# Optimization experiments

Measured on AMD Instinct MI355X. Metric: run time of the kernel, lower is better.

## Reference

```python
import jax, jax.numpy as jnp
import numpy as np

IN_DIM, HID_DIM, OUT_DIM, N_EXP = 3, 20, 3, 5
BATCH = 1 << 20


def setup_inputs() -> dict:
    key = jax.random.key(0)
    ks = jax.random.split(key, 8)
    s_in = 1.0 / np.sqrt(IN_DIM)
    s_hid = 1.0 / np.sqrt(HID_DIM)
    return {
        "x": jax.random.normal(ks[0], (BATCH, IN_DIM), dtype=jnp.float32),
        # stacked expert params: fc1 [E, in, hid], fc2 [E, hid, out]
        "W1": jax.random.uniform(ks[1], (N_EXP, IN_DIM, HID_DIM), jnp.float32, -s_in, s_in),
        "b1": jax.random.uniform(ks[2], (N_EXP, HID_DIM), jnp.float32, -s_in, s_in),
        "W2": jax.random.uniform(ks[3], (N_EXP, HID_DIM, OUT_DIM), jnp.float32, -s_hid, s_hid),
        "b2": jax.random.uniform(ks[4], (N_EXP, OUT_DIM), jnp.float32, -s_hid, s_hid),
        # gate Linear(in, n_experts)
        "Wg": jax.random.uniform(ks[5], (IN_DIM, N_EXP), jnp.float32, -s_in, s_in),
        "bg": jax.random.uniform(ks[6], (N_EXP,), jnp.float32, -s_in, s_in),
    }


def reference(x, W1, b1, W2, b2, Wg, bg):
    # all experts as one batched GEMM: h [B, E, hid]
    h = jax.nn.relu(jnp.einsum("bi,eih->beh", x, W1) + b1)
    expert_out = jnp.einsum("beh,eho->beo", h, W2) + b2  # [B, E, out]
    gate = jax.nn.softmax(x @ Wg + bg, axis=-1)           # [B, E]
    mixed = jnp.einsum("be,beo->bo", gate, expert_out)    # [B, out]
    return (mixed, gate)
```

## Files before the change

### kernel.cpp

```cpp
#include <hip/hip_runtime.h>

#define IN_DIM  3
#define HID_DIM 20
#define OUT_DIM 3
#define N_EXP   5
#define ELEMS   4
#define BLOCK   256
#define SPAN    (BLOCK * ELEMS)


__global__ __launch_bounds__(BLOCK) void moe_kernel(
    const float* __restrict__ x,
    const float* __restrict__ W1,
    const float* __restrict__ b1,
    const float* __restrict__ W2,
    const float* __restrict__ b2,
    const float* __restrict__ Wg,
    const float* __restrict__ bg,
    float* __restrict__ out,
    int B)
{
    __shared__ float sIO[SPAN * N_EXP];

    const int t = threadIdx.x;
    const long long blockBase = (long long)blockIdx.x * SPAN;
    float* __restrict__ mixed_out = out;
    float* __restrict__ gate_out  = out + (long long)B * OUT_DIM;

    if (blockBase + SPAN <= (long long)B) {
        const size_t bb = (size_t)blockBase;

        {
            const float4* g4 = reinterpret_cast<const float4*>(x + bb * IN_DIM);
            float4* s4 = reinterpret_cast<float4*>(sIO);
            #pragma unroll
            for (int k = 0; k < 3; ++k) s4[t + k * BLOCK] = g4[t + k * BLOCK];
        }
        __syncthreads();

        float xf[ELEMS * IN_DIM];
        {
            const float4* s4 = reinterpret_cast<const float4*>(sIO);
            #pragma unroll
            for (int k = 0; k < 3; ++k) {
                float4 v = s4[3 * t + k];
                xf[4 * k + 0] = v.x; xf[4 * k + 1] = v.y;
                xf[4 * k + 2] = v.z; xf[4 * k + 3] = v.w;
            }
        }
        __syncthreads();

        float gate[ELEMS][N_EXP];
        #pragma unroll
        for (int c = 0; c < ELEMS; ++c) {
            float lg[N_EXP]; float s = 0.f;
            #pragma unroll
            for (int e = 0; e < N_EXP; ++e) {
                float v = bg[e];
                #pragma unroll
                for (int i = 0; i < IN_DIM; ++i)
                    v = fmaf(xf[c * IN_DIM + i], Wg[i * N_EXP + e], v);
                v = __expf(v);
                lg[e] = v; s += v;
            }
            const float inv = 1.0f / s;
            #pragma unroll
            for (int e = 0; e < N_EXP; ++e) gate[c][e] = lg[e] * inv;
        }
        {
            float4* s4 = reinterpret_cast<float4*>(sIO);
            float g[ELEMS * N_EXP];
            #pragma unroll
            for (int c = 0; c < ELEMS; ++c)
                #pragma unroll
                for (int e = 0; e < N_EXP; ++e) g[c * N_EXP + e] = gate[c][e];
            #pragma unroll
            for (int k = 0; k < 5; ++k)
                s4[5 * t + k] = make_float4(g[4 * k + 0], g[4 * k + 1],
                                            g[4 * k + 2], g[4 * k + 3]);
        }
        __syncthreads();

        {
            float4* o4 = reinterpret_cast<float4*>(gate_out + bb * N_EXP);
            const float4* s4 = reinterpret_cast<const float4*>(sIO);
            #pragma unroll
            for (int k = 0; k < 5; ++k) o4[t + k * BLOCK] = s4[t + k * BLOCK];
        }

        float mix[ELEMS][OUT_DIM];
        #pragma unroll
        for (int c = 0; c < ELEMS; ++c) {
            #pragma unroll
            for (int k = 0; k < OUT_DIM; ++k) {
                float m = 0.f;
                #pragma unroll
                for (int e = 0; e < N_EXP; ++e)
                    m = fmaf(gate[c][e], b2[e * OUT_DIM + k], m);
                mix[c][k] = m;
            }
        }
        #pragma unroll
        for (int e = 0; e < N_EXP; ++e) {
            #pragma unroll
            for (int j = 0; j < HID_DIM; ++j) {
                const float w10 = W1[(e * IN_DIM + 0) * HID_DIM + j];
                const float w11 = W1[(e * IN_DIM + 1) * HID_DIM + j];
                const float w12 = W1[(e * IN_DIM + 2) * HID_DIM + j];
                const float bb1 = b1[e * HID_DIM + j];
                const float w20 = W2[(e * HID_DIM + j) * OUT_DIM + 0];
                const float w21 = W2[(e * HID_DIM + j) * OUT_DIM + 1];
                const float w22 = W2[(e * HID_DIM + j) * OUT_DIM + 2];
                #pragma unroll
                for (int c = 0; c < ELEMS; ++c) {
                    float h = fmaf(xf[c * IN_DIM + 2], w12,
                              fmaf(xf[c * IN_DIM + 1], w11,
                              fmaf(xf[c * IN_DIM + 0], w10, bb1)));
                    h = fmaxf(h, 0.f);
                    const float hg = h * gate[c][e];
                    mix[c][0] = fmaf(hg, w20, mix[c][0]);
                    mix[c][1] = fmaf(hg, w21, mix[c][1]);
                    mix[c][2] = fmaf(hg, w22, mix[c][2]);
                }
            }
        }
        __syncthreads();

        {
            float4* s4 = reinterpret_cast<float4*>(sIO);
            float m[ELEMS * OUT_DIM];
            #pragma unroll
            for (int c = 0; c < ELEMS; ++c)
                #pragma unroll
                for (int k = 0; k < OUT_DIM; ++k) m[c * OUT_DIM + k] = mix[c][k];
            #pragma unroll
            for (int k = 0; k < 3; ++k)
                s4[3 * t + k] = make_float4(m[4 * k + 0], m[4 * k + 1],
                                            m[4 * k + 2], m[4 * k + 3]);
        }
        __syncthreads();

        {
            float4* o4 = reinterpret_cast<float4*>(mixed_out + bb * OUT_DIM);
            const float4* s4 = reinterpret_cast<const float4*>(sIO);
            #pragma unroll
            for (int k = 0; k < 3; ++k) o4[t + k * BLOCK] = s4[t + k * BLOCK];
        }
    } else {
        for (int c = 0; c < ELEMS; ++c) {
            const long long bidx = blockBase + (long long)c * BLOCK + t;
            if (bidx >= (long long)B) continue;
            float xv[IN_DIM];
            for (int i = 0; i < IN_DIM; ++i) xv[i] = x[bidx * IN_DIM + i];

            float lg[N_EXP]; float s = 0.f;
            for (int e = 0; e < N_EXP; ++e) {
                float v = bg[e];
                for (int i = 0; i < IN_DIM; ++i)
                    v = fmaf(xv[i], Wg[i * N_EXP + e], v);
                v = __expf(v); lg[e] = v; s += v;
            }
            const float inv = 1.0f / s;
            for (int e = 0; e < N_EXP; ++e) lg[e] *= inv;

            float mixv[OUT_DIM] = {0.f, 0.f, 0.f};
            for (int e = 0; e < N_EXP; ++e) {
                for (int k = 0; k < OUT_DIM; ++k)
                    mixv[k] = fmaf(lg[e], b2[e * OUT_DIM + k], mixv[k]);
                for (int j = 0; j < HID_DIM; ++j) {
                    float h = b1[e * HID_DIM + j];
                    for (int i = 0; i < IN_DIM; ++i)
                        h = fmaf(xv[i], W1[(e * IN_DIM + i) * HID_DIM + j], h);
                    h = fmaxf(h, 0.f);
                    const float hg = h * lg[e];
                    for (int k = 0; k < OUT_DIM; ++k)
                        mixv[k] = fmaf(hg, W2[(e * HID_DIM + j) * OUT_DIM + k], mixv[k]);
                }
            }
            for (int k = 0; k < OUT_DIM; ++k)
                mixed_out[bidx * OUT_DIM + k] = mixv[k];
            for (int e = 0; e < N_EXP; ++e)
                gate_out[bidx * N_EXP + e] = lg[e];
        }
    }
}

extern "C" void kernel_launch(void* const* d_in, const int* in_sizes, int n_in,
                              void* d_out, int out_size, void* d_ws, size_t ws_size,
                              hipStream_t stream) {
    const float* x  = (const float*)d_in[0];
    const float* W1 = (const float*)d_in[1];
    const float* b1 = (const float*)d_in[2];
    const float* W2 = (const float*)d_in[3];
    const float* b2 = (const float*)d_in[4];
    const float* Wg = (const float*)d_in[5];
    const float* bg = (const float*)d_in[6];
    float* out = (float*)d_out;

    const int B = in_sizes[0] / IN_DIM;
    const int grid = (B + SPAN - 1) / SPAN;

    moe_kernel<<<grid, BLOCK, 0, stream>>>(x, W1, b1, W2, b2, Wg, bg, out, B);
}
```

Measured before the change: 109.0 us.

## Pack element pairs into float2 vectors and defer gate multiply per expert

```diff
diff --git a/kernel.cpp b/kernel.cpp
--- a/kernel.cpp
+++ b/kernel.cpp
@@ -5,9 +5,12 @@
 #define OUT_DIM 3
 #define N_EXP   5
 #define ELEMS   4
+#define PAIRS   (ELEMS / 2)
 #define BLOCK   256
 #define SPAN    (BLOCK * ELEMS)
 
+
+typedef float v2f __attribute__((ext_vector_type(2)));
 
 __global__ __launch_bounds__(BLOCK) void moe_kernel(
     const float* __restrict__ x,
@@ -38,42 +41,57 @@
         }
         __syncthreads();
 
-        float xf[ELEMS * IN_DIM];
+        v2f xp[PAIRS][IN_DIM];
         {
             const float4* s4 = reinterpret_cast<const float4*>(sIO);
+            float xf[ELEMS * IN_DIM];
             #pragma unroll
             for (int k = 0; k < 3; ++k) {
                 float4 v = s4[3 * t + k];
                 xf[4 * k + 0] = v.x; xf[4 * k + 1] = v.y;
                 xf[4 * k + 2] = v.z; xf[4 * k + 3] = v.w;
             }
-        }
-        __syncthreads();
-
-        float gate[ELEMS][N_EXP];
+            #pragma unroll
+            for (int p = 0; p < PAIRS; ++p)
+                #pragma unroll
+                for (int i = 0; i < IN_DIM; ++i)
+                    xp[p][i] = (v2f){xf[(2 * p) * IN_DIM + i],
+                                     (2 * p + 1) * IN_DIM + i < ELEMS * IN_DIM
+                                         ? xf[(2 * p + 1) * IN_DIM + i] : 0.f};
+        }
+        __syncthreads();
+
+        v2f gatep[PAIRS][N_EXP];
         #pragma unroll
-        for (int c = 0; c < ELEMS; ++c) {
-            float lg[N_EXP]; float s = 0.f;
+        for (int p = 0; p < PAIRS; ++p) {
+            v2f lg[N_EXP];
             #pragma unroll
             for (int e = 0; e < N_EXP; ++e) {
-                float v = bg[e];
-                #pragma unroll
-                for (int i = 0; i < IN_DIM; ++i)
-                    v = fmaf(xf[c * IN_DIM + i], Wg[i * N_EXP + e], v);
-                v = __expf(v);
-                lg[e] = v; s += v;
-            }
-            const float inv = 1.0f / s;
-            #pragma unroll
-            for (int e = 0; e < N_EXP; ++e) gate[c][e] = lg[e] * inv;
+                v2f v = (v2f){bg[e], bg[e]};
+                #pragma unroll
+                for (int i = 0; i < IN_DIM; ++i) {
+                    const float w = Wg[i * N_EXP + e];
+                    v = __builtin_elementwise_fma(xp[p][i], (v2f){w, w}, v);
+                }
+                lg[e] = (v2f){__expf(v.x), __expf(v.y)};
+            }
+            v2f s = (v2f){0.f, 0.f};
+            #pragma unroll
+            for (int e = 0; e < N_EXP; ++e) s += lg[e];
+            const v2f inv = (v2f){1.0f / s.x, 1.0f / s.y};
+            #pragma unroll
+            for (int e = 0; e < N_EXP; ++e) gatep[p][e] = lg[e] * inv;
         }
         {
             float4* s4 = reinterpret_cast<float4*>(sIO);
             float g[ELEMS * N_EXP];
             #pragma unroll
-            for (int c = 0; c < ELEMS; ++c)
-                #pragma unroll
-                for (int e = 0; e < N_EXP; ++e) g[c * N_EXP + e] = gate[c][e];
+            for (int p = 0; p < PAIRS; ++p)
+                #pragma unroll
+                for (int e = 0; e < N_EXP; ++e) {
+                    g[(2 * p) * N_EXP + e]     = gatep[p][e].x;
+                    g[(2 * p + 1) * N_EXP + e] = gatep[p][e].y;
+                }
             #pragma unroll
             for (int k = 0; k < 5; ++k)
                 s4[5 * t + k] = make_float4(g[4 * k + 0], g[4 * k + 1],
@@ -88,20 +106,22 @@
             for (int k = 0; k < 5; ++k) o4[t + k * BLOCK] = s4[t + k * BLOCK];
         }
 
-        float mix[ELEMS][OUT_DIM];
+        v2f mix[PAIRS][OUT_DIM];
         #pragma unroll
-        for (int c = 0; c < ELEMS; ++c) {
-            #pragma unroll
-            for (int k = 0; k < OUT_DIM; ++k) {
-                float m = 0.f;
-                #pragma unroll
-                for (int e = 0; e < N_EXP; ++e)
-                    m = fmaf(gate[c][e], b2[e * OUT_DIM + k], m);
-                mix[c][k] = m;
-            }
-        }
+        for (int p = 0; p < PAIRS; ++p)
+            #pragma unroll
+            for (int k = 0; k < OUT_DIM; ++k) mix[p][k] = (v2f){0.f, 0.f};
+
         #pragma unroll
         for (int e = 0; e < N_EXP; ++e) {
+            v2f oacc[PAIRS][OUT_DIM];
+            #pragma unroll
+            for (int p = 0; p < PAIRS; ++p)
+                #pragma unroll
+                for (int k = 0; k < OUT_DIM; ++k) {
+                    const float bk = b2[e * OUT_DIM + k];
+                    oacc[p][k] = (v2f){bk, bk};
+                }
             #pragma unroll
             for (int j = 0; j < HID_DIM; ++j) {
                 const float w10 = W1[(e * IN_DIM + 0) * HID_DIM + j];
@@ -111,18 +131,27 @@
                 const float w20 = W2[(e * HID_DIM + j) * OUT_DIM + 0];
                 const float w21 = W2[(e * HID_DIM + j) * OUT_DIM + 1];
                 const float w22 = W2[(e * HID_DIM + j) * OUT_DIM + 2];
-                #pragma unroll
-                for (int c = 0; c < ELEMS; ++c) {
-                    float h = fmaf(xf[c * IN_DIM + 2], w12,
-                              fmaf(xf[c * IN_DIM + 1], w11,
-                              fmaf(xf[c * IN_DIM + 0], w10, bb1)));
-                    h = fmaxf(h, 0.f);
-                    const float hg = h * gate[c][e];
-                    mix[c][0] = fmaf(hg, w20, mix[c][0]);
-                    mix[c][1] = fmaf(hg, w21, mix[c][1]);
-                    mix[c][2] = fmaf(hg, w22, mix[c][2]);
-                }
-            }
+                const v2f w10v = (v2f){w10, w10}, w11v = (v2f){w11, w11};
+                const v2f w12v = (v2f){w12, w12}, bb1v = (v2f){bb1, bb1};
+                const v2f w20v = (v2f){w20, w20}, w21v = (v2f){w21, w21};
+                const v2f w22v = (v2f){w22, w22};
+                #pragma unroll
+                for (int p = 0; p < PAIRS; ++p) {
+                    v2f h = __builtin_elementwise_fma(xp[p][2], w12v,
+                            __builtin_elementwise_fma(xp[p][1], w11v,
+                            __builtin_elementwise_fma(xp[p][0], w10v, bb1v)));
+                    h = __builtin_elementwise_max(h, (v2f){0.f, 0.f});
+                    oacc[p][0] = __builtin_elementwise_fma(h, w20v, oacc[p][0]);
+                    oacc[p][1] = __builtin_elementwise_fma(h, w21v, oacc[p][1]);
+                    oacc[p][2] = __builtin_elementwise_fma(h, w22v, oacc[p][2]);
+                }
+            }
+            #pragma unroll
+            for (int p = 0; p < PAIRS; ++p)
+                #pragma unroll
+                for (int k = 0; k < OUT_DIM; ++k)
+                    mix[p][k] = __builtin_elementwise_fma(gatep[p][e], oacc[p][k],
+                                                          mix[p][k]);
         }
         __syncthreads();
 
@@ -130,9 +159,12 @@
             float4* s4 = reinterpret_cast<float4*>(sIO);
             float m[ELEMS * OUT_DIM];
             #pragma unroll
-            for (int c = 0; c < ELEMS; ++c)
-                #pragma unroll
-                for (int k = 0; k < OUT_DIM; ++k) m[c * OUT_DIM + k] = mix[c][k];
+            for (int p = 0; p < PAIRS; ++p)
+                #pragma unroll
+                for (int k = 0; k < OUT_DIM; ++k) {
+                    m[(2 * p) * OUT_DIM + k]     = mix[p][k].x;
+                    m[(2 * p + 1) * OUT_DIM + k] = mix[p][k].y;
+                }
             #pragma unroll
             for (int k = 0; k < 3; ++k)
                 s4[3 * t + k] = make_float4(m[4 * k + 0], m[4 * k + 1],
```

Result: faster. 98.66 us (-9.4%).

## Pack two rows per thread into float2 vectors and defer gate multiply per expert

Applied to the files above, without the earlier changes.

```diff
diff --git a/kernel.cpp b/kernel.cpp
--- a/kernel.cpp
+++ b/kernel.cpp
@@ -4,10 +4,12 @@
 #define HID_DIM 20
 #define OUT_DIM 3
 #define N_EXP   5
-#define ELEMS   4
+#define ELEMS   2
 #define BLOCK   256
 #define SPAN    (BLOCK * ELEMS)
 
+
+typedef float v2f __attribute__((ext_vector_type(2)));
 
 __global__ __launch_bounds__(BLOCK) void moe_kernel(
     const float* __restrict__ x,
@@ -33,75 +35,75 @@
         {
             const float4* g4 = reinterpret_cast<const float4*>(x + bb * IN_DIM);
             float4* s4 = reinterpret_cast<float4*>(sIO);
-            #pragma unroll
-            for (int k = 0; k < 3; ++k) s4[t + k * BLOCK] = g4[t + k * BLOCK];
-        }
-        __syncthreads();
-
-        float xf[ELEMS * IN_DIM];
-        {
-            const float4* s4 = reinterpret_cast<const float4*>(sIO);
-            #pragma unroll
-            for (int k = 0; k < 3; ++k) {
-                float4 v = s4[3 * t + k];
-                xf[4 * k + 0] = v.x; xf[4 * k + 1] = v.y;
-                xf[4 * k + 2] = v.z; xf[4 * k + 3] = v.w;
-            }
-        }
-        __syncthreads();
-
-        float gate[ELEMS][N_EXP];
-        #pragma unroll
-        for (int c = 0; c < ELEMS; ++c) {
-            float lg[N_EXP]; float s = 0.f;
+            s4[t] = g4[t];
+            if (t < (SPAN * IN_DIM) / 4 - BLOCK)
+                s4[t + BLOCK] = g4[t + BLOCK];
+        }
+        __syncthreads();
+
+        v2f xp[IN_DIM];
+        {
+            const float2* s2 = reinterpret_cast<const float2*>(sIO);
+            float2 a = s2[3 * t + 0];
+            float2 b = s2[3 * t + 1];
+            float2 c = s2[3 * t + 2];
+            xp[0] = (v2f){a.x, b.y};
+            xp[1] = (v2f){a.y, c.x};
+            xp[2] = (v2f){b.x, c.y};
+        }
+        __syncthreads();
+
+        v2f gatep[N_EXP];
+        {
+            v2f lg[N_EXP];
             #pragma unroll
             for (int e = 0; e < N_EXP; ++e) {
-                float v = bg[e];
+                v2f v = (v2f){bg[e], bg[e]};
                 #pragma unroll
-                for (int i = 0; i < IN_DIM; ++i)
-                    v = fmaf(xf[c * IN_DIM + i], Wg[i * N_EXP + e], v);
-                v = __expf(v);
-                lg[e] = v; s += v;
-            }
-            const float inv = 1.0f / s;
-            #pragma unroll
-            for (int e = 0; e < N_EXP; ++e) gate[c][e] = lg[e] * inv;
-        }
-        {
-            float4* s4 = reinterpret_cast<float4*>(sIO);
-            float g[ELEMS * N_EXP];
-            #pragma unroll
-            for (int c = 0; c < ELEMS; ++c)
-                #pragma unroll
-                for (int e = 0; e < N_EXP; ++e) g[c * N_EXP + e] = gate[c][e];
-            #pragma unroll
-            for (int k = 0; k < 5; ++k)
-                s4[5 * t + k] = make_float4(g[4 * k + 0], g[4 * k + 1],
-                                            g[4 * k + 2], g[4 * k + 3]);
+                for (int i = 0; i < IN_DIM; ++i) {
+                    const float w = Wg[i * N_EXP + e];
+                    v = __builtin_elementwise_fma(xp[i], (v2f){w, w}, v);
+                }
+                lg[e] = (v2f){__expf(v.x), __expf(v.y)};
+            }
+            v2f s = (v2f){0.f, 0.f};
+            #pragma unroll
+            for (int e = 0; e < N_EXP; ++e) s += lg[e];
+            const v2f inv = (v2f){1.0f / s.x, 1.0f / s.y};
+            #pragma unroll
+            for (int e = 0; e < N_EXP; ++e) gatep[e] = lg[e] * inv;
+        }
+        {
+            float2* s2 = reinterpret_cast<float2*>(sIO);
+            s2[5 * t + 0] = make_float2(gatep[0].x, gatep[1].x);
+            s2[5 * t + 1] = make_float2(gatep[2].x, gatep[3].x);
+            s2[5 * t + 2] = make_float2(gatep[4].x, gatep[0].y);
+            s2[5 * t + 3] = make_float2(gatep[1].y, gatep[2].y);
+            s2[5 * t + 4] = make_float2(gatep[3].y, gatep[4].y);
         }
         __syncthreads();
 
         {
             float4* o4 = reinterpret_cast<float4*>(gate_out + bb * N_EXP);
             const float4* s4 = reinterpret_cast<const float4*>(sIO);
-            #pragma unroll
-            for (int k = 0; k < 5; ++k) o4[t + k * BLOCK] = s4[t + k * BLOCK];
-        }
-
-        float mix[ELEMS][OUT_DIM];
+            o4[t] = s4[t];
+            o4[t + BLOCK] = s4[t + BLOCK];
+            if (t < (SPAN * N_EXP) / 4 - 2 * BLOCK)
+                o4[t + 2 * BLOCK] = s4[t + 2 * BLOCK];
+        }
+
+        v2f mix[OUT_DIM];
         #pragma unroll
-        for (int c = 0; c < ELEMS; ++c) {
-            #pragma unroll
-            for (int k = 0; k < OUT_DIM; ++k) {
-                float m = 0.f;
-                #pragma unroll
-                for (int e = 0; e < N_EXP; ++e)
-                    m = fmaf(gate[c][e], b2[e * OUT_DIM + k], m);
-                mix[c][k] = m;
-            }
-        }
+        for (int k = 0; k < OUT_DIM; ++k) mix[k] = (v2f){0.f, 0.f};
+
         #pragma unroll
         for (int e = 0; e < N_EXP; ++e) {
+            v2f oacc[OUT_DIM];
+            #pragma unroll
+            for (int k = 0; k < OUT_DIM; ++k) {
+                const float bk = b2[e * OUT_DIM + k];
+                oacc[k] = (v2f){bk, bk};
+            }
             #pragma unroll
             for (int j = 0; j < HID_DIM; ++j) {
                 const float w10 = W1[(e * IN_DIM + 0) * HID_DIM + j];
@@ -111,40 +113,35 @@
                 const float w20 = W2[(e * HID_DIM + j) * OUT_DIM + 0];
                 const float w21 = W2[(e * HID_DIM + j) * OUT_DIM + 1];
                 const float w22 = W2[(e * HID_DIM + j) * OUT_DIM + 2];
-                #pragma unroll
-                for (int c = 0; c < ELEMS; ++c) {
-                    float h = fmaf(xf[c * IN_DIM + 2], w12,
-                              fmaf(xf[c * IN_DIM + 1], w11,
-                              fmaf(xf[c * IN_DIM + 0], w10, bb1)));
-                    h = fmaxf(h, 0.f);
-                    const float hg = h * gate[c][e];
-                    mix[c][0] = fmaf(hg, w20, mix[c][0]);
-                    mix[c][1] = fmaf(hg, w21, mix[c][1]);
-                    mix[c][2] = fmaf(hg, w22, mix[c][2]);
-                }
-            }
-        }
-        __syncthreads();
-
-        {
-            float4* s4 = reinterpret_cast<float4*>(sIO);
-            float m[ELEMS * OUT_DIM];
-            #pragma unroll
-            for (int c = 0; c < ELEMS; ++c)
-                #pragma unroll
-                for (int k = 0; k < OUT_DIM; ++k) m[c * OUT_DIM + k] = mix[c][k];
-            #pragma unroll
-            for (int k = 0; k < 3; ++k)
-                s4[3 * t + k] = make_float4(m[4 * k + 0], m[4 * k + 1],
-                                            m[4 * k + 2], m[4 * k + 3]);
+                v2f h = __builtin_elementwise_fma(xp[2], (v2f){w12, w12},
+                        __builtin_elementwise_fma(xp[1], (v2f){w11, w11},
+                        __builtin_elementwise_fma(xp[0], (v2f){w10, w10},
+                                                  (v2f){bb1, bb1})));
+                h = __builtin_elementwise_max(h, (v2f){0.f, 0.f});
+                oacc[0] = __builtin_elementwise_fma(h, (v2f){w20, w20}, oacc[0]);
+                oacc[1] = __builtin_elementwise_fma(h, (v2f){w21, w21}, oacc[1]);
+                oacc[2] = __builtin_elementwise_fma(h, (v2f){w22, w22}, oacc[2]);
+            }
+            #pragma unroll
+            for (int k = 0; k < OUT_DIM; ++k)
+                mix[k] = __builtin_elementwise_fma(gatep[e], oacc[k], mix[k]);
+        }
+        __syncthreads();
+
+        {
+            float2* s2 = reinterpret_cast<float2*>(sIO);
+            s2[3 * t + 0] = make_float2(mix[0].x, mix[1].x);
+            s2[3 * t + 1] = make_float2(mix[2].x, mix[0].y);
+            s2[3 * t + 2] = make_float2(mix[1].y, mix[2].y);
         }
         __syncthreads();
 
         {
             float4* o4 = reinterpret_cast<float4*>(mixed_out + bb * OUT_DIM);
             const float4* s4 = reinterpret_cast<const float4*>(sIO);
-            #pragma unroll
-            for (int k = 0; k < 3; ++k) o4[t + k * BLOCK] = s4[t + k * BLOCK];
+            o4[t] = s4[t];
+            if (t < (SPAN * OUT_DIM) / 4 - BLOCK)
+                o4[t + BLOCK] = s4[t + BLOCK];
         }
     } else {
         for (int c = 0; c < ELEMS; ++c) {
```

New measurement: 100.6 us. 1.08x faster.
